# Kernel optimization log

Measured on AMD Instinct MI355X. Metric: run time of the kernel, lower is better.

Reference implementation:

```python
import jax, jax.numpy as jnp
import numpy as np

N = 50000
E = 800000
EQ = 200000
IN_DIM = 256
H1 = 256
H2 = 128
EA = 16


def _lrelu(x):
    return jax.nn.leaky_relu(x, negative_slope=0.01)


def gcn_conv(h, edge_index, W, b, num_nodes):
    # PyG GCNConv: add self-loops, symmetric normalization, out = A_hat (h W) + b
    row, col = edge_index[0], edge_index[1]
    loop = jnp.arange(num_nodes, dtype=row.dtype)
    row = jnp.concatenate([row, loop])
    col = jnp.concatenate([col, loop])
    deg = jax.ops.segment_sum(jnp.ones(row.shape[0], dtype=h.dtype), col, num_segments=num_nodes)
    dinv = jnp.where(deg > 0, jax.lax.rsqrt(deg), 0.0)
    norm = dinv[row] * dinv[col]                      # [E+N]
    hw = h @ W                                        # [N, out]
    msg = hw[row] * norm[:, None]                     # gather + scale
    out = jax.ops.segment_sum(msg, col, num_segments=num_nodes)
    return out + b


def gru_cell(x, h, Wih, Whh, bih, bhh):
    # torch.nn.GRUCell, gate order (r, z, n); Wih/Whh stored as [in, 3H]
    gi = x @ Wih + bih
    gh = h @ Whh + bhh
    ir, iz, inn = jnp.split(gi, 3, axis=1)
    hr, hz, hn = jnp.split(gh, 3, axis=1)
    r = jax.nn.sigmoid(ir + hr)
    z = jax.nn.sigmoid(iz + hz)
    n = jnp.tanh(inn + r * hn)
    return (1.0 - z) * n + z * h


def setup_inputs() -> dict:
    key = jax.random.key(0)
    ks = jax.random.split(key, 24)

    def gn(k, shape, scale=0.05):
        return (jax.random.normal(k, shape, dtype=jnp.float32) * scale)

    inp = {
        "x": jax.random.normal(ks[0], (N, IN_DIM), dtype=jnp.float32),
        "edge_index": jax.random.randint(ks[1], (2, E), 0, N, dtype=jnp.int32).astype(jnp.int64),
        "edge_label_index": jax.random.randint(ks[2], (2, EQ), 0, N, dtype=jnp.int32).astype(jnp.int64),
        "edge_attr": jax.random.normal(ks[3], (EQ, EA), dtype=jnp.float32),
        "prev1": jax.random.normal(ks[4], (N, H1), dtype=jnp.float32) * 0.1,
        "prev2": jax.random.normal(ks[5], (N, H2), dtype=jnp.float32) * 0.1,
        "pre1_W": gn(ks[6], (IN_DIM, 256)), "pre1_b": jnp.zeros((256,), jnp.float32),
        "pre2_W": gn(ks[7], (256, 128)), "pre2_b": jnp.zeros((128,), jnp.float32),
        "conv1_W": gn(ks[8], (128, H1)), "conv1_b": jnp.zeros((H1,), jnp.float32),
        "conv2_W": gn(ks[9], (H1, H2)), "conv2_b": jnp.zeros((H2,), jnp.float32),
        "gru1_Wih": gn(ks[10], (H1, 3 * H1)), "gru1_Whh": gn(ks[11], (H1, 3 * H1)),
        "gru1_bih": jnp.zeros((3 * H1,), jnp.float32), "gru1_bhh": jnp.zeros((3 * H1,), jnp.float32),
        "gru2_Wih": gn(ks[12], (H2, 3 * H2)), "gru2_Whh": gn(ks[13], (H2, 3 * H2)),
        "gru2_bih": jnp.zeros((3 * H2,), jnp.float32), "gru2_bhh": jnp.zeros((3 * H2,), jnp.float32),
        "post_W": gn(ks[14], (2 * H2 + EA, 1)), "post_b": jnp.zeros((1,), jnp.float32),
    }
    return inp


def reference(x, edge_index, edge_label_index, edge_attr, prev1, prev2,
              pre1_W, pre1_b, pre2_W, pre2_b,
              conv1_W, conv1_b, conv2_W, conv2_b,
              gru1_Wih, gru1_Whh, gru1_bih, gru1_bhh,
              gru2_Wih, gru2_Whh, gru2_bih, gru2_bhh,
              post_W, post_b):
    num_nodes = x.shape[0]
    # dense preprocessing (dropout p=0.0 -> identity)
    h = _lrelu(x @ pre1_W + pre1_b)
    h = _lrelu(h @ pre2_W + pre2_b)          # [N,128]
    # GCN layer 1 + GRU update with previous embeddings
    h = _lrelu(gcn_conv(h, edge_index, conv1_W, conv1_b, num_nodes))
    h = gru_cell(h, prev1, gru1_Wih, gru1_Whh, gru1_bih, gru1_bhh)
    emb1 = h
    # GCN layer 2 + GRU update
    h = _lrelu(gcn_conv(h, edge_index, conv2_W, conv2_b, num_nodes))
    h = gru_cell(h, prev2, gru2_Wih, gru2_Whh, gru2_bih, gru2_bhh)
    emb2 = h
    # edge-level prediction: gather endpoints, concat with edge_attr, linear
    h_src = h[edge_label_index[0]]
    h_dst = h[edge_label_index[1]]
    combined = jnp.concatenate([h_src, h_dst, edge_attr], axis=1)  # [Eq, 2*H2+EA]
    scores = (combined @ post_W + post_b).reshape(-1)              # [Eq]
    return (scores, emb1, emb2)
```

## Files before the change

kernel.cpp:

```cpp
#include <hip/hip_runtime.h>
#include <hip/hip_bf16.h>

#define DEVFN __device__ __forceinline__

constexpr int NN = 50000;
constexpr int NE = 800000;
constexpr int NQ = 200000;
constexpr long MP = 50048;

typedef __attribute__((ext_vector_type(8))) short bf16x8;
typedef __attribute__((ext_vector_type(2))) short s16x2;
typedef __attribute__((ext_vector_type(2))) float f32x2;
typedef __attribute__((ext_vector_type(4))) float f32x4;
typedef __attribute__((address_space(1))) const void gv_t;
typedef __attribute__((address_space(3))) void lv_t;

DEVFN float lrelu(float x) { return x > 0.f ? x : 0.01f * x; }
DEVFN float sigmoidf(float x) { return 1.f / (1.f + __expf(-x)); }
DEVFN float tanh_fast(float x) {
    float xc = fminf(fmaxf(x, -15.f), 15.f);
    float t = __expf(2.f * xc);
    return (t - 1.f) / (t + 1.f);
}

DEVFN short f2b(float v) {
    __hip_bfloat16 h = __float2bfloat16(v);
    return *reinterpret_cast<short*>(&h);
}
DEVFN float b2f(short s) {
    union { unsigned u; float f; } z;
    z.u = ((unsigned)(unsigned short)s) << 16;
    return z.f;
}
DEVFN void gld16(const void* g, void* l) {
    __builtin_amdgcn_global_load_lds((gv_t*)g, (lv_t*)l, 16, 0, 0);
}

#define WAITV4 asm volatile("s_waitcnt vmcnt(4)" ::: "memory")
#define WAITV0 asm volatile("s_waitcnt vmcnt(0)" ::: "memory")
#define CFENCE asm volatile("" ::: "memory")

DEVFN void swz_rc(int d, int nwg, int NC, int& rw, int& cs) {
    int q0 = nwg >> 3, rr = nwg & 7;
    int xcd = d & 7, idx = d >> 3;
    int w = (xcd < rr ? xcd * (q0 + 1) : rr * (q0 + 1) + (xcd - rr) * q0) + idx;
    rw = w / NC;
    cs = w - rw * NC;
}

template <int H>
DEVFN float gruw_val(const float* Wih, const float* Whh, int i) {
    constexpr int K2 = 2 * H, W3 = 3 * H;
    int np = i / K2, k = i % K2;
    int g16 = np >> 6, chunk = (np >> 4) & 3, cl = np & 15;
    int c = g16 * 16 + cl;
    if (chunk == 0) return (k < H) ? Wih[(long)k * W3 + c] : Whh[(long)(k - H) * W3 + c];
    if (chunk == 1) return (k < H) ? Wih[(long)k * W3 + H + c] : Whh[(long)(k - H) * W3 + H + c];
    if (chunk == 2) return (k < H) ? Wih[(long)k * W3 + 2 * H + c] : 0.f;
    return (k < H) ? 0.f : Whh[(long)(k - H) * W3 + 2 * H + c];
}

constexpr long U_XB   = MP * 256 / 8;
constexpr long U_PREV = (long)NN * 256 / 8;
constexpr long U_CNT  = NE;
constexpr long U_P1T  = 65536 / 8;
constexpr long U_P2T  = 32768 / 8;
constexpr long U_C1T  = 32768 / 8;
constexpr long U_C2T  = 32768 / 8;
constexpr long U_W1   = 524288 / 8;
constexpr long U_W2   = 131072 / 8;
constexpr long U_TOT  = U_XB + U_PREV + U_CNT + U_P1T + U_P2T + U_C1T + U_C2T + U_W1 + U_W2;

__global__ void prep_all(const float* __restrict__ x, const float* __restrict__ prev1,
                         const float* __restrict__ pre1W, const float* __restrict__ pre2W,
                         const float* __restrict__ conv1W, const float* __restrict__ conv2W,
                         const float* __restrict__ g1ih, const float* __restrict__ g1hh,
                         const float* __restrict__ g2ih, const float* __restrict__ g2hh,
                         const int* __restrict__ cols, int* __restrict__ cnt,
                         short* __restrict__ xb, short* __restrict__ AP1,
                         short* __restrict__ pre1T, short* __restrict__ pre2T,
                         short* __restrict__ conv1T, short* __restrict__ conv2T,
                         short* __restrict__ W1g1, short* __restrict__ W1g2) {
    long i = (long)blockIdx.x * 256 + threadIdx.x;
    if (i < U_XB) {
        long base = i * 8;
        bf16x8 o;
        if (base < (long)NN * 256) {
            f32x4 a = *(const f32x4*)&x[base];
            f32x4 b = *(const f32x4*)&x[base + 4];
#pragma unroll
            for (int j = 0; j < 4; ++j) { o[j] = f2b(a[j]); o[4 + j] = f2b(b[j]); }
        } else {
            o = bf16x8{0, 0, 0, 0, 0, 0, 0, 0};
        }
        *(bf16x8*)&xb[base] = o;
        return;
    }
    i -= U_XB;
    if (i < U_PREV) {
        long base = i * 8;
        long r = base >> 8;
        int c = (int)(base & 255);
        f32x4 a = *(const f32x4*)&prev1[base];
        f32x4 b = *(const f32x4*)&prev1[base + 4];
        bf16x8 o;
#pragma unroll
        for (int j = 0; j < 4; ++j) { o[j] = f2b(a[j]); o[4 + j] = f2b(b[j]); }
        *(bf16x8*)&AP1[r * 512 + 256 + c] = o;
        return;
    }
    i -= U_PREV;
    if (i < U_CNT) { atomicAdd(&cnt[cols[i]], 1); return; }
    i -= U_CNT;
    if (i < U_P1T) {
        int ii = (int)i * 8, n = ii >> 8, k = ii & 255;
        bf16x8 o;
#pragma unroll
        for (int j = 0; j < 8; ++j) o[j] = f2b(pre1W[(k + j) * 256 + n]);
        *(bf16x8*)&pre1T[ii] = o;
        return;
    }
    i -= U_P1T;
    if (i < U_P2T) {
        int ii = (int)i * 8, n = ii >> 8, k = ii & 255;
        bf16x8 o;
#pragma unroll
        for (int j = 0; j < 8; ++j) o[j] = f2b(pre2W[(k + j) * 128 + n]);
        *(bf16x8*)&pre2T[ii] = o;
        return;
    }
    i -= U_P2T;
    if (i < U_C1T) {
        int ii = (int)i * 8, n = ii >> 7, k = ii & 127;
        bf16x8 o;
#pragma unroll
        for (int j = 0; j < 8; ++j) o[j] = f2b(conv1W[(k + j) * 256 + n]);
        *(bf16x8*)&conv1T[ii] = o;
        return;
    }
    i -= U_C1T;
    if (i < U_C2T) {
        int ii = (int)i * 8, n = ii >> 8, k = ii & 255;
        bf16x8 o;
#pragma unroll
        for (int j = 0; j < 8; ++j) o[j] = f2b(conv2W[(k + j) * 128 + n]);
        *(bf16x8*)&conv2T[ii] = o;
        return;
    }
    i -= U_C2T;
    if (i < U_W1) {
        int ii = (int)i * 8;
        bf16x8 o;
#pragma unroll
        for (int j = 0; j < 8; ++j) o[j] = f2b(gruw_val<256>(g1ih, g1hh, ii + j));
        *(bf16x8*)&W1g1[ii] = o;
        return;
    }
    i -= U_W1;
    if (i < U_W2) {
        int ii = (int)i * 8;
        bf16x8 o;
#pragma unroll
        for (int j = 0; j < 8; ++j) o[j] = f2b(gruw_val<128>(g2ih, g2hh, ii + j));
        *(bf16x8*)&W1g2[ii] = o;
    }
}

template <int EPI, int K>
__global__ __launch_bounds__(256)
void gemm_mfma(const short* __restrict__ A, const short* __restrict__ Bt,
               const float* __restrict__ bias,
               short* __restrict__ Cb, int obS, int NC, int nwg) {
    constexpr int NS = K / 32;
    __shared__ alignas(16) short As[3][4096];
    __shared__ alignas(16) short Bs[3][4096];
    const int tid = threadIdx.x;
    const int lane = tid & 63, w = tid >> 6;
    const int wr = w >> 1, wc = w & 1;
    int rw, cs;
    swz_rc(blockIdx.x, nwg, NC, rw, cs);
    const long row0 = (long)rw * 128;
    const long col0 = (long)cs * 128;

    f32x4 acc[4][4] = {};

    const int kcs = ((tid & 3) ^ ((tid >> 3) & 3)) * 8;
    const short* gA = A + (row0 + (tid >> 2)) * (long)K + kcs;
    const short* gB = Bt + (col0 + (tid >> 2)) * (long)K + kcs;
    const long half = 64 * (long)K;

    auto stage = [&](int b, int k0) {
        gld16(gA + k0, &As[b][tid * 8]);
        gld16(gA + half + k0, &As[b][2048 + tid * 8]);
        gld16(gB + k0, &Bs[b][tid * 8]);
        gld16(gB + half + k0, &Bs[b][2048 + tid * 8]);
    };

    stage(0, 0);
    stage(1, 32);
    const int l15 = lane & 15;
    const int kq = ((lane >> 4) ^ ((l15 >> 1) & 3)) * 8;
#pragma unroll
    for (int t = 0; t < NS; ++t) {
        if (t + 1 < NS) { WAITV4; } else { WAITV0; }
        __builtin_amdgcn_s_barrier();
        CFENCE;
        if (t + 2 < NS) stage((t + 2) % 3, (t + 2) * 32);
        const int cur = t % 3;
        bf16x8 af[4], bfr[4];
#pragma unroll
        for (int i = 0; i < 4; ++i)
            af[i] = *(const bf16x8*)&As[cur][(wr * 64 + i * 16 + l15) * 32 + kq];
#pragma unroll
        for (int j = 0; j < 4; ++j)
            bfr[j] = *(const bf16x8*)&Bs[cur][(wc * 64 + j * 16 + l15) * 32 + kq];
#pragma unroll
        for (int i = 0; i < 4; ++i)
#pragma unroll
            for (int j = 0; j < 4; ++j)
                acc[i][j] = __builtin_amdgcn_mfma_f32_16x16x32_bf16(af[i], bfr[j], acc[i][j], 0, 0, 0);
    }

    const int cr = (lane >> 4) * 4, cc = lane & 15;
#pragma unroll
    for (int i = 0; i < 4; ++i) {
#pragma unroll
        for (int j = 0; j < 4; ++j) {
            const long col = col0 + wc * 64 + j * 16 + cc;
            float bv = (EPI == 1) ? bias[col] : 0.f;
#pragma unroll
            for (int r = 0; r < 4; ++r) {
                const long row = row0 + wr * 64 + i * 16 + cr + r;
                float v = acc[i][j][r];
                if (EPI == 1) v = lrelu(v + bv);
                Cb[row * obS + col] = f2b(v);
            }
        }
    }
}

template <int H, bool WRITEB>
__global__ __launch_bounds__(256)
void gru_wide(const short* __restrict__ AP, const short* __restrict__ W1,
              const float* __restrict__ prevf,
              const float* __restrict__ bih, const float* __restrict__ bhh,
              float* __restrict__ outF, short* __restrict__ outB, int M,
              int NC, int nwg) {
    constexpr int K2 = 2 * H;
    constexpr int NS = K2 / 32;
    __shared__ alignas(16) short As[3][4096];
    __shared__ alignas(16) short Bs[3][4096];
    const int tid = threadIdx.x;
    const int lane = tid & 63, w = tid >> 6;
    const int wr = w >> 1, wc = w & 1;
    int rw, cs;
    swz_rc(blockIdx.x, nwg, NC, rw, cs);
    const long row0 = (long)rw * 128;

    f32x4 acc[4][4] = {};

    const int kcs = ((tid & 3) ^ ((tid >> 3) & 3)) * 8;
    const short* gA = AP + (row0 + (tid >> 2)) * (long)K2 + kcs;
    const short* gB = W1 + ((long)cs * 128 + (tid >> 2)) * (long)K2 + kcs;
    const long half = 64 * (long)K2;

    auto stage = [&](int b, int k0) {
        gld16(gA + k0, &As[b][tid * 8]);
        gld16(gA + half + k0, &As[b][2048 + tid * 8]);
        gld16(gB + k0, &Bs[b][tid * 8]);
        gld16(gB + half + k0, &Bs[b][2048 + tid * 8]);
    };

    stage(0, 0);
    stage(1, 32);
    const int l15 = lane & 15;
    const int kq = ((lane >> 4) ^ ((l15 >> 1) & 3)) * 8;
#pragma unroll
    for (int t = 0; t < NS; ++t) {
        const bool lo = (t * 32 < H);
        if (t + 1 < NS) { WAITV4; } else { WAITV0; }
        __builtin_amdgcn_s_barrier();
        CFENCE;
        if (t + 2 < NS) stage((t + 2) % 3, (t + 2) * 32);
        const int cur = t % 3;
        bf16x8 af[4], bfr[4];
#pragma unroll
        for (int i = 0; i < 4; ++i)
            af[i] = *(const bf16x8*)&As[cur][(wr * 64 + i * 16 + l15) * 32 + kq];
#pragma unroll
        for (int j = 0; j < 4; ++j) {
            if ((j == 2 && !lo) || (j == 3 && lo)) continue;
            bfr[j] = *(const bf16x8*)&Bs[cur][(wc * 64 + j * 16 + l15) * 32 + kq];
        }
#pragma unroll
        for (int i = 0; i < 4; ++i)
#pragma unroll
            for (int j = 0; j < 4; ++j) {
                if ((j == 2 && !lo) || (j == 3 && lo)) continue;
                acc[i][j] = __builtin_amdgcn_mfma_f32_16x16x32_bf16(af[i], bfr[j], acc[i][j], 0, 0, 0);
            }
    }

    const int cr = (lane >> 4) * 4;
    const int c = cs * 32 + wc * 16 + (lane & 15);
    const float bsr = bih[c] + bhh[c];
    const float bsz = bih[H + c] + bhh[H + c];
    const float bin = bih[2 * H + c];
    const float bhn = bhh[2 * H + c];
#pragma unroll
    for (int i = 0; i < 4; ++i) {
#pragma unroll
        for (int r = 0; r < 4; ++r) {
            const long row = row0 + wr * 64 + i * 16 + cr + r;
            if (row >= M) continue;
            float rg = sigmoidf(acc[i][0][r] + bsr);
            float zg = sigmoidf(acc[i][1][r] + bsz);
            float ng = tanh_fast(acc[i][2][r] + bin + rg * (acc[i][3][r] + bhn));
            float o = (1.f - zg) * ng + zg * prevf[row * (long)H + c];
            outF[row * (long)H + c] = o;
            if (WRITEB) outB[row * (long)H + c] = f2b(o);
        }
    }
}

__global__ void scan1(const int* __restrict__ cnt, int* __restrict__ off,
                      int* __restrict__ bsum, float* __restrict__ dinv, int n) {
    __shared__ int sm[256];
    int i = blockIdx.x * 256 + threadIdx.x;
    int v = (i < n) ? cnt[i] : 0;
    if (i < n) dinv[i] = rsqrtf((float)v + 1.0f);
    sm[threadIdx.x] = v;
    __syncthreads();
    for (int s = 1; s < 256; s <<= 1) {
        int t = (threadIdx.x >= s) ? sm[threadIdx.x - s] : 0;
        __syncthreads();
        sm[threadIdx.x] += t;
        __syncthreads();
    }
    if (i < n) off[i + 1] = sm[threadIdx.x];
    if (threadIdx.x == 255) bsum[blockIdx.x] = sm[255];
}

__global__ void scan2(int* __restrict__ bsum, int nb) {
    __shared__ int sm[256];
    int v = (threadIdx.x < nb) ? bsum[threadIdx.x] : 0;
    sm[threadIdx.x] = v;
    __syncthreads();
    for (int s = 1; s < 256; s <<= 1) {
        int t = (threadIdx.x >= s) ? sm[threadIdx.x - s] : 0;
        __syncthreads();
        sm[threadIdx.x] += t;
        __syncthreads();
    }
    if (threadIdx.x < nb) bsum[threadIdx.x] = sm[threadIdx.x] - v;
}

__global__ void scan3(int* __restrict__ off, const int* __restrict__ bsum, int n) {
    int i = blockIdx.x * 256 + threadIdx.x;
    if (i < n) off[i + 1] += bsum[blockIdx.x];
    if (i == 0) off[0] = 0;
}

__global__ void fill_csr(const int* __restrict__ rows, const int* __restrict__ cols,
                         const float* __restrict__ dinv, const int* __restrict__ off,
                         int* __restrict__ cursor, int* __restrict__ srow,
                         float* __restrict__ snorm, int E) {
    int e = blockIdx.x * 256 + threadIdx.x;
    if (e >= E) return;
    int r = rows[e], c = cols[e];
    int p = off[c] + atomicAdd(&cursor[c], 1);
    srow[p] = r;
    snorm[p] = dinv[r] * dinv[c];
}

template <int OS, bool EPI, bool PREV>
__global__ __launch_bounds__(256)
void gather_agg(const short* __restrict__ hwb, const int* __restrict__ off,
                const int* __restrict__ srow, const float* __restrict__ snorm,
                const float* __restrict__ dinv, const float* __restrict__ bias,
                const float* __restrict__ prevf,
                short* __restrict__ aggb, int n) {
    constexpr int H = 128;
    int t = blockIdx.x * 256 + threadIdx.x;
    int c = t >> 6, l = t & 63;
    if (c >= n) return;
    const int fo = l * 2;
    float acc0, acc1;
    {
        float dd = dinv[c] * dinv[c];
        s16x2 v = *(const s16x2*)&hwb[(long)c * H + fo];
        acc0 = b2f(v[0]) * dd;
        acc1 = b2f(v[1]) * dd;
    }
    int e = off[c];
    const int e1 = off[c + 1];
    for (; e + 3 < e1; e += 4) {
        int r0 = srow[e], r1 = srow[e + 1], r2 = srow[e + 2], r3 = srow[e + 3];
        float n0 = snorm[e], n1 = snorm[e + 1], n2 = snorm[e + 2], n3 = snorm[e + 3];
        s16x2 v0 = *(const s16x2*)&hwb[(long)r0 * H + fo];
        s16x2 v1 = *(const s16x2*)&hwb[(long)r1 * H + fo];
        s16x2 v2 = *(const s16x2*)&hwb[(long)r2 * H + fo];
        s16x2 v3 = *(const s16x2*)&hwb[(long)r3 * H + fo];
        acc0 += b2f(v0[0]) * n0 + b2f(v1[0]) * n1 + b2f(v2[0]) * n2 + b2f(v3[0]) * n3;
        acc1 += b2f(v0[1]) * n0 + b2f(v1[1]) * n1 + b2f(v2[1]) * n2 + b2f(v3[1]) * n3;
    }
    for (; e < e1; ++e) {
        int r0 = srow[e];
        float n0 = snorm[e];
        s16x2 v0 = *(const s16x2*)&hwb[(long)r0 * H + fo];
        acc0 += b2f(v0[0]) * n0;
        acc1 += b2f(v0[1]) * n0;
    }
    s16x2 o;
    if (EPI) {
        o[0] = f2b(lrelu(acc0 + bias[fo]));
        o[1] = f2b(lrelu(acc1 + bias[fo + 1]));
    } else {
        o[0] = f2b(acc0);
        o[1] = f2b(acc1);
    }
    *(s16x2*)&aggb[(long)c * OS + fo] = o;
    if (PREV) {
        f32x2 p = *(const f32x2*)&prevf[(long)c * H + fo];
        s16x2 pb;
        pb[0] = f2b(p[0]);
        pb[1] = f2b(p[1]);
        *(s16x2*)&aggb[(long)c * OS + H + fo] = pb;
    }
}

__global__ void node_dots(const short* __restrict__ emb2b, const float* __restrict__ pw,
                          float* __restrict__ u, float* __restrict__ v, int n) {
    int t = blockIdx.x * 256 + threadIdx.x;
    int c = t >> 6, l = t & 63;
    if (c >= n) return;
    const int f = l * 2;
    s16x2 e = *(const s16x2*)&emb2b[(long)c * 128 + f];
    float e0 = b2f(e[0]), e1 = b2f(e[1]);
    float ua = e0 * pw[f] + e1 * pw[f + 1];
    float va = e0 * pw[128 + f] + e1 * pw[128 + f + 1];
#pragma unroll
    for (int off = 32; off > 0; off >>= 1) {
        ua += __shfl_down(ua, off);
        va += __shfl_down(va, off);
    }
    if (l == 0) { u[c] = ua; v[c] = va; }
}

__global__ void edge_lite(const int* __restrict__ eli, const float* __restrict__ ea,
                          const float* __restrict__ pw, const float* __restrict__ pb,
                          const float* __restrict__ u, const float* __restrict__ v,
                          float* __restrict__ scores, int Q) {
    int t = blockIdx.x * 256 + threadIdx.x;
    int e = t >> 4, l = t & 15;
    if (e >= Q) return;
    float acc = ea[(long)e * 16 + l] * pw[256 + l];
#pragma unroll
    for (int off = 8; off > 0; off >>= 1) acc += __shfl_down(acc, off, 16);
    if (l == 0) {
        int s = eli[e], d = eli[Q + e];
        scores[e] = acc + u[s] + v[d] + pb[0];
    }
}


extern "C" void kernel_launch(void* const* d_in, const int* in_sizes, int n_in,
                              void* d_out, int out_size, void* d_ws, size_t ws_size,
                              hipStream_t stream) {
    const float* x       = (const float*)d_in[0];
    const int*   ei      = (const int*)d_in[1];
    const int*   eli     = (const int*)d_in[2];
    const float* eattr   = (const float*)d_in[3];
    const float* prev1   = (const float*)d_in[4];
    const float* prev2   = (const float*)d_in[5];
    const float* pre1_W  = (const float*)d_in[6];
    const float* pre1_b  = (const float*)d_in[7];
    const float* pre2_W  = (const float*)d_in[8];
    const float* pre2_b  = (const float*)d_in[9];
    const float* conv1_W = (const float*)d_in[10];
    const float* conv1_b = (const float*)d_in[11];
    const float* conv2_W = (const float*)d_in[12];
    const float* conv2_b = (const float*)d_in[13];
    const float* g1_Wih  = (const float*)d_in[14];
    const float* g1_Whh  = (const float*)d_in[15];
    const float* g1_bih  = (const float*)d_in[16];
    const float* g1_bhh  = (const float*)d_in[17];
    const float* g2_Wih  = (const float*)d_in[18];
    const float* g2_Whh  = (const float*)d_in[19];
    const float* g2_bih  = (const float*)d_in[20];
    const float* g2_bhh  = (const float*)d_in[21];
    const float* post_W  = (const float*)d_in[22];
    const float* post_b  = (const float*)d_in[23];

    float* out    = (float*)d_out;
    float* scores = out;
    float* emb1   = out + NQ;
    float* emb2   = emb1 + (long)NN * 256;

    char* ws = (char*)d_ws;
    const long S256 = MP * 256 * 2;
    const long S128 = MP * 128 * 2;
    short* R1  = (short*)ws;
    short* R2  = (short*)(ws + S256);
    short* R3  = (short*)(ws + 2 * S256);
    short* AP1 = (short*)(ws + 2 * S256 + S128);
    short* AP2 = R1;
    char*  wts = ws + 4 * S256 + S128;
    short* pre1T  = (short*)wts;
    short* pre2T  = pre1T + 256 * 256;
    short* conv1T = pre2T + 128 * 256;
    short* conv2T = conv1T + 256 * 128;
    short* W1g1   = conv2T + 128 * 256;
    short* W1g2   = W1g1 + 1024 * 512;
    float* dinv   = (float*)(W1g2 + 512 * 256);
    int*   cnt    = (int*)(dinv + NN);
    int*   cursor = cnt + NN;
    int*   off    = cursor + NN;
    int*   bsum   = off + NN + 1;
    int*   srow   = bsum + 256;
    float* snorm  = (float*)(srow + NE);
    float* uvec   = snorm + NE;
    float* vvec   = uvec + NN;

    const int* rows = ei;
    const int* cols = ei + NE;

    dim3 blk(256);
    const int NB = (NN + 255) / 256;

    hipMemsetAsync(cnt, 0, 2 * NN * sizeof(int), stream);
    prep_all<<<(int)((U_TOT + 255) / 256), blk, 0, stream>>>(
        x, prev1, pre1_W, pre2_W, conv1_W, conv2_W,
        g1_Wih, g1_Whh, g2_Wih, g2_Whh, cols, cnt,
        R1, AP1, pre1T, pre2T, conv1T, conv2T, W1g1, W1g2);

    scan1<<<NB, blk, 0, stream>>>(cnt, off, bsum, dinv, NN);
    scan2<<<1, blk, 0, stream>>>(bsum, NB);
    scan3<<<NB, blk, 0, stream>>>(off, bsum, NN);
    fill_csr<<<(NE + 255) / 256, blk, 0, stream>>>(rows, cols, dinv, off, cursor, srow, snorm, NE);

    gemm_mfma<1, 256><<<782, blk, 0, stream>>>(R1, pre1T, pre1_b, R2, 256, 2, 782);
    gemm_mfma<1, 256><<<391, blk, 0, stream>>>(R2, pre2T, pre2_b, R3, 128, 1, 391);

    gather_agg<128, false, false><<<(NN + 3) / 4, blk, 0, stream>>>(
        R3, off, srow, snorm, dinv, nullptr, nullptr, R1, NN);
    gemm_mfma<1, 128><<<782, blk, 0, stream>>>(R1, conv1T, conv1_b, AP1, 512, 2, 782);

    gru_wide<256, true><<<3128, blk, 0, stream>>>(AP1, W1g1, prev1, g1_bih, g1_bhh,
                                                  emb1, R2, NN, 8, 3128);

    gemm_mfma<0, 256><<<391, blk, 0, stream>>>(R2, conv2T, nullptr, R3, 128, 1, 391);

    gather_agg<256, true, true><<<(NN + 3) / 4, blk, 0, stream>>>(
        R3, off, srow, snorm, dinv, conv2_b, prev2, AP2, NN);

    gru_wide<128, true><<<1564, blk, 0, stream>>>(AP2, W1g2, prev2, g2_bih, g2_bhh,
                                                  emb2, R3, NN, 4, 1564);

    node_dots<<<(NN + 3) / 4, blk, 0, stream>>>(R3, post_W, uvec, vvec, NN);
    edge_lite<<<(NQ + 15) / 16, blk, 0, stream>>>(eli, eattr, post_W, post_b,
                                                  uvec, vvec, scores, NQ);
}
```

Measured before the change: 414.8 us.

## Use 64-row tiles for N=128 GEMMs, raise MFMA priority, read prev state from bf16 AP

Adds a BM template parameter to the MFMA GEMM so the two 128-column-output GEMMs use 64-row tiles, doubling the workgroup count from 391 to 782 to fill more CUs. The vmcnt wait is adjusted to match the smaller A stage. s_setprio is raised around MFMA blocks in both the GEMM and GRU kernels to favour matrix issue. The GRU epilogue now reads the previous hidden state from the bf16 copy packed into AP instead of the fp32 prev tensor, which cuts memory traffic but lowers the precision of the z*h term.

```diff
diff --git a/kernel.cpp b/kernel.cpp
--- a/kernel.cpp
+++ b/kernel.cpp
@@ -36,6 +36,7 @@
     __builtin_amdgcn_global_load_lds((gv_t*)g, (lv_t*)l, 16, 0, 0);
 }
 
+#define WAITV3 asm volatile("s_waitcnt vmcnt(3)" ::: "memory")
 #define WAITV4 asm volatile("s_waitcnt vmcnt(4)" ::: "memory")
 #define WAITV0 asm volatile("s_waitcnt vmcnt(0)" ::: "memory")
 #define CFENCE asm volatile("" ::: "memory")
@@ -166,34 +167,37 @@
     }
 }
 
-template <int EPI, int K>
+template <int EPI, int K, int BM>
 __global__ __launch_bounds__(256)
 void gemm_mfma(const short* __restrict__ A, const short* __restrict__ Bt,
                const float* __restrict__ bias,
                short* __restrict__ Cb, int obS, int NC, int nwg) {
     constexpr int NS = K / 32;
-    __shared__ alignas(16) short As[3][4096];
+    constexpr int AQ = BM / 64;
+    constexpr int RF = BM / 32;
+    __shared__ alignas(16) short As[3][BM * 32];
     __shared__ alignas(16) short Bs[3][4096];
     const int tid = threadIdx.x;
     const int lane = tid & 63, w = tid >> 6;
     const int wr = w >> 1, wc = w & 1;
     int rw, cs;
     swz_rc(blockIdx.x, nwg, NC, rw, cs);
-    const long row0 = (long)rw * 128;
+    const long row0 = (long)rw * BM;
     const long col0 = (long)cs * 128;
 
-    f32x4 acc[4][4] = {};
+    f32x4 acc[RF][4] = {};
 
     const int kcs = ((tid & 3) ^ ((tid >> 3) & 3)) * 8;
     const short* gA = A + (row0 + (tid >> 2)) * (long)K + kcs;
     const short* gB = Bt + (col0 + (tid >> 2)) * (long)K + kcs;
-    const long half = 64 * (long)K;
+    const long h64 = 64 * (long)K;
 
     auto stage = [&](int b, int k0) {
-        gld16(gA + k0, &As[b][tid * 8]);
-        gld16(gA + half + k0, &As[b][2048 + tid * 8]);
+#pragma unroll
+        for (int q = 0; q < AQ; ++q)
+            gld16(gA + q * h64 + k0, &As[b][q * 2048 + tid * 8]);
         gld16(gB + k0, &Bs[b][tid * 8]);
-        gld16(gB + half + k0, &Bs[b][2048 + tid * 8]);
+        gld16(gB + h64 + k0, &Bs[b][2048 + tid * 8]);
     };
 
     stage(0, 0);
@@ -202,35 +206,39 @@
     const int kq = ((lane >> 4) ^ ((l15 >> 1) & 3)) * 8;
 #pragma unroll
     for (int t = 0; t < NS; ++t) {
-        if (t + 1 < NS) { WAITV4; } else { WAITV0; }
+        if (t + 1 < NS) {
+            if constexpr (AQ == 1) { WAITV3; } else { WAITV4; }
+        } else { WAITV0; }
         __builtin_amdgcn_s_barrier();
         CFENCE;
         if (t + 2 < NS) stage((t + 2) % 3, (t + 2) * 32);
         const int cur = t % 3;
-        bf16x8 af[4], bfr[4];
-#pragma unroll
-        for (int i = 0; i < 4; ++i)
-            af[i] = *(const bf16x8*)&As[cur][(wr * 64 + i * 16 + l15) * 32 + kq];
+        bf16x8 af[RF], bfr[4];
+#pragma unroll
+        for (int i = 0; i < RF; ++i)
+            af[i] = *(const bf16x8*)&As[cur][(wr * (BM / 2) + i * 16 + l15) * 32 + kq];
 #pragma unroll
         for (int j = 0; j < 4; ++j)
             bfr[j] = *(const bf16x8*)&Bs[cur][(wc * 64 + j * 16 + l15) * 32 + kq];
-#pragma unroll
-        for (int i = 0; i < 4; ++i)
+        __builtin_amdgcn_s_setprio(1);
+#pragma unroll
+        for (int i = 0; i < RF; ++i)
 #pragma unroll
             for (int j = 0; j < 4; ++j)
                 acc[i][j] = __builtin_amdgcn_mfma_f32_16x16x32_bf16(af[i], bfr[j], acc[i][j], 0, 0, 0);
+        __builtin_amdgcn_s_setprio(0);
     }
 
     const int cr = (lane >> 4) * 4, cc = lane & 15;
 #pragma unroll
-    for (int i = 0; i < 4; ++i) {
+    for (int i = 0; i < RF; ++i) {
 #pragma unroll
         for (int j = 0; j < 4; ++j) {
             const long col = col0 + wc * 64 + j * 16 + cc;
             float bv = (EPI == 1) ? bias[col] : 0.f;
 #pragma unroll
             for (int r = 0; r < 4; ++r) {
-                const long row = row0 + wr * 64 + i * 16 + cr + r;
+                const long row = row0 + wr * (BM / 2) + i * 16 + cr + r;
                 float v = acc[i][j][r];
                 if (EPI == 1) v = lrelu(v + bv);
                 Cb[row * obS + col] = f2b(v);
@@ -242,7 +250,6 @@
 template <int H, bool WRITEB>
 __global__ __launch_bounds__(256)
 void gru_wide(const short* __restrict__ AP, const short* __restrict__ W1,
-              const float* __restrict__ prevf,
               const float* __restrict__ bih, const float* __restrict__ bhh,
               float* __restrict__ outF, short* __restrict__ outB, int M,
               int NC, int nwg) {
@@ -292,6 +299,7 @@
             if ((j == 2 && !lo) || (j == 3 && lo)) continue;
             bfr[j] = *(const bf16x8*)&Bs[cur][(wc * 64 + j * 16 + l15) * 32 + kq];
         }
+        __builtin_amdgcn_s_setprio(1);
 #pragma unroll
         for (int i = 0; i < 4; ++i)
 #pragma unroll
@@ -299,6 +307,7 @@
                 if ((j == 2 && !lo) || (j == 3 && lo)) continue;
                 acc[i][j] = __builtin_amdgcn_mfma_f32_16x16x32_bf16(af[i], bfr[j], acc[i][j], 0, 0, 0);
             }
+        __builtin_amdgcn_s_setprio(0);
     }
 
     const int cr = (lane >> 4) * 4;
@@ -316,7 +325,8 @@
             float rg = sigmoidf(acc[i][0][r] + bsr);
             float zg = sigmoidf(acc[i][1][r] + bsz);
             float ng = tanh_fast(acc[i][2][r] + bin + rg * (acc[i][3][r] + bhn));
-            float o = (1.f - zg) * ng + zg * prevf[row * (long)H + c];
+            float pv = b2f(AP[row * (long)K2 + H + c]);
+            float o = (1.f - zg) * ng + zg * pv;
             outF[row * (long)H + c] = o;
             if (WRITEB) outB[row * (long)H + c] = f2b(o);
         }
@@ -539,22 +549,22 @@
     scan3<<<NB, blk, 0, stream>>>(off, bsum, NN);
     fill_csr<<<(NE + 255) / 256, blk, 0, stream>>>(rows, cols, dinv, off, cursor, srow, snorm, NE);
 
-    gemm_mfma<1, 256><<<782, blk, 0, stream>>>(R1, pre1T, pre1_b, R2, 256, 2, 782);
-    gemm_mfma<1, 256><<<391, blk, 0, stream>>>(R2, pre2T, pre2_b, R3, 128, 1, 391);
+    gemm_mfma<1, 256, 128><<<782, blk, 0, stream>>>(R1, pre1T, pre1_b, R2, 256, 2, 782);
+    gemm_mfma<1, 256, 64><<<782, blk, 0, stream>>>(R2, pre2T, pre2_b, R3, 128, 1, 782);
 
     gather_agg<128, false, false><<<(NN + 3) / 4, blk, 0, stream>>>(
         R3, off, srow, snorm, dinv, nullptr, nullptr, R1, NN);
-    gemm_mfma<1, 128><<<782, blk, 0, stream>>>(R1, conv1T, conv1_b, AP1, 512, 2, 782);
-
-    gru_wide<256, true><<<3128, blk, 0, stream>>>(AP1, W1g1, prev1, g1_bih, g1_bhh,
+    gemm_mfma<1, 128, 128><<<782, blk, 0, stream>>>(R1, conv1T, conv1_b, AP1, 512, 2, 782);
+
+    gru_wide<256, true><<<3128, blk, 0, stream>>>(AP1, W1g1, g1_bih, g1_bhh,
                                                   emb1, R2, NN, 8, 3128);
 
-    gemm_mfma<0, 256><<<391, blk, 0, stream>>>(R2, conv2T, nullptr, R3, 128, 1, 391);
+    gemm_mfma<0, 256, 64><<<782, blk, 0, stream>>>(R2, conv2T, nullptr, R3, 128, 1, 782);
 
     gather_agg<256, true, true><<<(NN + 3) / 4, blk, 0, stream>>>(
         R3, off, srow, snorm, dinv, conv2_b, prev2, AP2, NN);
 
-    gru_wide<128, true><<<1564, blk, 0, stream>>>(AP2, W1g2, prev2, g2_bih, g2_bhh,
+    gru_wide<128, true><<<1564, blk, 0, stream>>>(AP2, W1g2, g2_bih, g2_bhh,
                                                   emb2, R3, NN, 4, 1564);
 
     node_dots<<<(NN + 3) / 4, blk, 0, stream>>>(R3, post_W, uvec, vvec, NN);
```

After: 393.0 us. -5.3%, faster.
